# Kernel tuning notes

Hardware: AMD Instinct MI355X
Metric: run time of the kernel (lower is better)

The kernel has to match this reference:

```python
import jax, jax.numpy as jnp
import numpy as np

N = 100_000        # node_num
E_RAND = 1_600_000 # random edges; self-loops appended (PyG add_self_loops=True)
F_IN = 128         # n_xdims
HEADS = 8          # gat_nhead
F_HID = 8          # GATConv out_channels of layer 1
SLOPE = 0.2        # PyG GATConv default negative_slope


def _gat_layer(x, src, dst, W, a_src, a_dst, bias, heads, out_dim, n):
    # x: [N, Fin], W: [Fin, heads*out_dim], a_*: [heads, out_dim], bias: [heads*out_dim]
    h = (x @ W).reshape(n, heads, out_dim)                 # [N, H, D]
    s = jnp.sum(h * a_src, axis=-1)                        # [N, H] per-node src term
    d = jnp.sum(h * a_dst, axis=-1)                        # [N, H] per-node dst term
    e = jax.nn.leaky_relu(s[src] + d[dst], SLOPE)          # [E, H] edge logits
    # segment softmax over incoming edges of each destination node
    m = jax.ops.segment_max(e, dst, num_segments=n)        # [N, H]
    ex = jnp.exp(e - m[dst])                               # [E, H]
    denom = jax.ops.segment_sum(ex, dst, num_segments=n)   # [N, H]
    alpha = ex / denom[dst]                                # [E, H]
    msg = h[src] * alpha[:, :, None]                       # [E, H, D]
    out = jax.ops.segment_sum(msg, dst, num_segments=n)    # [N, H, D]
    return out.reshape(n, heads * out_dim) + bias          # concat=True


def setup_inputs() -> dict:
    key = jax.random.key(0)
    ks = jax.random.split(key, 10)
    x = jax.random.normal(ks[0], (N, F_IN), dtype=jnp.float32)
    ei = jax.random.randint(ks[1], (2, E_RAND), 0, N, dtype=jnp.int64)
    loops = jnp.broadcast_to(jnp.arange(N, dtype=jnp.int64), (2, N))
    edge_index = jnp.concatenate([ei, loops], axis=1)      # [2, E_RAND + N]
    g1 = 1.0 / np.sqrt(F_IN)
    g2 = 1.0 / np.sqrt(HEADS * F_HID)
    return {
        "x": x,
        "edge_index": edge_index,
        "W1": jax.random.normal(ks[2], (F_IN, HEADS * F_HID), dtype=jnp.float32) * g1,
        "a_src1": jax.random.normal(ks[3], (HEADS, F_HID), dtype=jnp.float32) * g2,
        "a_dst1": jax.random.normal(ks[4], (HEADS, F_HID), dtype=jnp.float32) * g2,
        "b1": jnp.zeros((HEADS * F_HID,), dtype=jnp.float32),
        "W2": jax.random.normal(ks[5], (HEADS * F_HID, F_IN), dtype=jnp.float32) * g2,
        "a_src2": jax.random.normal(ks[6], (1, F_IN), dtype=jnp.float32) * (1.0 / np.sqrt(F_IN)),
        "a_dst2": jax.random.normal(ks[7], (1, F_IN), dtype=jnp.float32) * (1.0 / np.sqrt(F_IN)),
        "b2": jnp.zeros((F_IN,), dtype=jnp.float32),
    }


def reference(x, edge_index, W1, a_src1, a_dst1, b1, W2, a_src2, a_dst2, b2):
    src, dst = edge_index[0], edge_index[1]
    h = _gat_layer(x, src, dst, W1, a_src1, a_dst1, b1, HEADS, F_HID, N)
    h = jax.nn.relu(h)
    out = _gat_layer(h, src, dst, W2, a_src2, a_dst2, b2, 1, F_IN, N)
    return out
```

## Files before the change

kernel.cpp:

```cpp
#include <hip/hip_runtime.h>
#include <math.h>


#define SORT_EPB 4096

static __device__ __forceinline__ float lrelu(float v) {
    return v > 0.f ? v : 0.2f * v;
}

__global__ __launch_bounds__(64) void k_w2a(const float* __restrict__ W2,
                                            const float* __restrict__ as2,
                                            const float* __restrict__ ad2,
                                            float* __restrict__ w2as,
                                            float* __restrict__ w2ad) {
    int k = threadIdx.x;
    const float* row = W2 + k * 128;
    float s = 0.f, d = 0.f;
    #pragma unroll 8
    for (int j = 0; j < 128; ++j) { s = fmaf(row[j], as2[j], s); d = fmaf(row[j], ad2[j], d); }
    w2as[k] = s; w2ad[k] = d;
}

__global__ __launch_bounds__(256) void k_scan_blocks(const int* __restrict__ deg,
                                                     int* __restrict__ offs,
                                                     int* __restrict__ bsum, int N) {
    __shared__ int ls[256];
    const int t = threadIdx.x;
    const int base = blockIdx.x * 1024 + t * 4;
    int v0 = (base + 0 < N) ? deg[base + 0] : 0;
    int v1 = (base + 1 < N) ? deg[base + 1] : 0;
    int v2 = (base + 2 < N) ? deg[base + 2] : 0;
    int v3 = (base + 3 < N) ? deg[base + 3] : 0;
    const int sum = v0 + v1 + v2 + v3;
    int val = sum;
    ls[t] = val;
    __syncthreads();
    for (int off = 1; off < 256; off <<= 1) {
        int x = (t >= off) ? ls[t - off] : 0;
        __syncthreads();
        val += x;
        ls[t] = val;
        __syncthreads();
    }
    int run = val - sum;
    if (base + 0 < N) offs[base + 0] = run;  run += v0;
    if (base + 1 < N) offs[base + 1] = run;  run += v1;
    if (base + 2 < N) offs[base + 2] = run;  run += v2;
    if (base + 3 < N) offs[base + 3] = run;
    if (t == 255) bsum[blockIdx.x] = val;
}

__global__ __launch_bounds__(256) void k_scan_tops(int* __restrict__ bsum, int B) {
    __shared__ int ls[256];
    const int t = threadIdx.x;
    int v = (t < B) ? bsum[t] : 0;
    int val = v;
    ls[t] = val;
    __syncthreads();
    for (int off = 1; off < 256; off <<= 1) {
        int x = (t >= off) ? ls[t - off] : 0;
        __syncthreads();
        val += x;
        ls[t] = val;
        __syncthreads();
    }
    if (t < B) bsum[t] = val - v;
}

__global__ __launch_bounds__(256) void k_scan_add(int* __restrict__ offs,
                                                  const int* __restrict__ bsum,
                                                  int N, int E) {
    int i = blockIdx.x * 256 + threadIdx.x;
    if (i < N) offs[i] = offs[i] + bsum[i >> 10];
    if (i == 0) offs[N] = E;
}

__global__ __launch_bounds__(256) void k_hist(const int* __restrict__ dst,
                                              int* __restrict__ counts,
                                              int E, int B, int NB2) {
    __shared__ int h[256];
    const int t = threadIdx.x;
    const int b = blockIdx.x;
    h[t] = 0;
    __syncthreads();
    const int base_i = b * SORT_EPB;
    #pragma unroll 4
    for (int k = 0; k < 16; ++k) {
        int i = base_i + k * 256 + t;
        if (i < E) atomicAdd(&h[dst[i] >> 9], 1);
    }
    __syncthreads();
    if (t < NB2) counts[t * B + b] = h[t];
}

__global__ __launch_bounds__(256) void k_bucket_scatter(const int* __restrict__ src,
                                                        const int* __restrict__ dst,
                                                        const int* __restrict__ base,
                                                        int* __restrict__ packed,
                                                        int E, int B, int NB2) {
    __shared__ int cur[256];
    const int t = threadIdx.x;
    const int b = blockIdx.x;
    if (t < NB2) cur[t] = base[t * B + b];
    __syncthreads();
    const int base_i = b * SORT_EPB;
    #pragma unroll 4
    for (int k = 0; k < 16; ++k) {
        int i = base_i + k * 256 + t;
        if (i < E) {
            int d = dst[i];
            int pos = atomicAdd(&cur[d >> 9], 1);
            packed[pos] = (src[i] << 9) | (d & 511);
        }
    }
}

__global__ __launch_bounds__(256) void k_bucket_sort(const int* __restrict__ packed,
                                                     const int* __restrict__ base,
                                                     int* __restrict__ srcs,
                                                     int* __restrict__ offs,
                                                     int E, int B, int N) {
    __shared__ int h[512], sc[512], cur[512], ls[256];
    const int t = threadIdx.x;
    const int j = blockIdx.x;
    const int bstart = base[j * B];
    const int bend   = base[(j + 1) * B];
    h[t] = 0; h[t + 256] = 0;
    __syncthreads();
    for (int i = bstart + t; i < bend; i += 256)
        atomicAdd(&h[packed[i] & 511], 1);
    __syncthreads();
    const int a0 = h[2 * t], a1 = h[2 * t + 1];
    int val = a0 + a1;
    ls[t] = val;
    __syncthreads();
    for (int off = 1; off < 256; off <<= 1) {
        int x = (t >= off) ? ls[t - off] : 0;
        __syncthreads();
        val += x;
        ls[t] = val;
        __syncthreads();
    }
    const int pre = val - (a0 + a1);
    sc[2 * t] = pre;         sc[2 * t + 1] = pre + a0;
    cur[2 * t] = pre;        cur[2 * t + 1] = pre + a0;
    __syncthreads();
    const int node0 = j * 512 + 2 * t;
    if (node0 < N)     offs[node0]     = bstart + sc[2 * t];
    if (node0 + 1 < N) offs[node0 + 1] = bstart + sc[2 * t + 1];
    if (j == 0 && t == 0) offs[N] = E;
    for (int i = bstart + t; i < bend; i += 256) {
        int p = packed[i];
        int pos = atomicAdd(&cur[p & 511], 1);
        srcs[bstart + pos] = p >> 9;
    }
}

__global__ __launch_bounds__(256) void k_gemm1(const float* __restrict__ x,
                                               const float* __restrict__ W,
                                               const float* __restrict__ a_s,
                                               const float* __restrict__ a_d,
                                               float* __restrict__ h,
                                               float* __restrict__ s1,
                                               float* __restrict__ d1, int N) {
    __shared__ float Ws[128 * 64];
    __shared__ float xs[64][68];
    const int t = threadIdx.x;
    for (int i = t; i < 128 * 64; i += 256) Ws[i] = W[i];
    const int row0 = blockIdx.x * 64;
    const int tc = (t & 15) * 4;
    const int tr = (t >> 4) * 4;
    float acc[4][4] = {};
    for (int kb = 0; kb < 128; kb += 64) {
        if (kb) __syncthreads();
        for (int i = t; i < 1024; i += 256) {
            int r = i >> 4, c = i & 15;
            float4 v = make_float4(0.f, 0.f, 0.f, 0.f);
            if (row0 + r < N)
                v = *(const float4*)(x + (size_t)(row0 + r) * 128 + kb + c * 4);
            *(float4*)&xs[r][c * 4] = v;
        }
        __syncthreads();
        #pragma unroll 4
        for (int k = 0; k < 64; k += 4) {
            const float4 xv0 = *(const float4*)&xs[tr + 0][k];
            const float4 xv1 = *(const float4*)&xs[tr + 1][k];
            const float4 xv2 = *(const float4*)&xs[tr + 2][k];
            const float4 xv3 = *(const float4*)&xs[tr + 3][k];
            #pragma unroll
            for (int kk = 0; kk < 4; ++kk) {
                const float4 w = *(const float4*)&Ws[(kb + k + kk) * 64 + tc];
                const float a0 = (&xv0.x)[kk], a1 = (&xv1.x)[kk];
                const float a2 = (&xv2.x)[kk], a3 = (&xv3.x)[kk];
                acc[0][0] = fmaf(a0, w.x, acc[0][0]); acc[0][1] = fmaf(a0, w.y, acc[0][1]);
                acc[0][2] = fmaf(a0, w.z, acc[0][2]); acc[0][3] = fmaf(a0, w.w, acc[0][3]);
                acc[1][0] = fmaf(a1, w.x, acc[1][0]); acc[1][1] = fmaf(a1, w.y, acc[1][1]);
                acc[1][2] = fmaf(a1, w.z, acc[1][2]); acc[1][3] = fmaf(a1, w.w, acc[1][3]);
                acc[2][0] = fmaf(a2, w.x, acc[2][0]); acc[2][1] = fmaf(a2, w.y, acc[2][1]);
                acc[2][2] = fmaf(a2, w.z, acc[2][2]); acc[2][3] = fmaf(a2, w.w, acc[2][3]);
                acc[3][0] = fmaf(a3, w.x, acc[3][0]); acc[3][1] = fmaf(a3, w.y, acc[3][1]);
                acc[3][2] = fmaf(a3, w.z, acc[3][2]); acc[3][3] = fmaf(a3, w.w, acc[3][3]);
            }
        }
    }
    #pragma unroll
    for (int i = 0; i < 4; ++i) {
        int r = row0 + tr + i;
        if (r < N)
            *(float4*)(h + (size_t)r * 64 + tc) =
                make_float4(acc[i][0], acc[i][1], acc[i][2], acc[i][3]);
    }
    const float as0 = a_s[tc + 0], as1v = a_s[tc + 1], as2v = a_s[tc + 2], as3 = a_s[tc + 3];
    const float ad0 = a_d[tc + 0], ad1v = a_d[tc + 1], ad2v = a_d[tc + 2], ad3 = a_d[tc + 3];
    #pragma unroll
    for (int i = 0; i < 4; ++i) {
        float ps = acc[i][0] * as0 + acc[i][1] * as1v + acc[i][2] * as2v + acc[i][3] * as3;
        float pd = acc[i][0] * ad0 + acc[i][1] * ad1v + acc[i][2] * ad2v + acc[i][3] * ad3;
        ps += __shfl_xor(ps, 1);
        pd += __shfl_xor(pd, 1);
        int r = row0 + tr + i;
        if ((t & 1) == 0 && r < N) {
            int hh = (t & 15) >> 1;
            s1[r * 8 + hh] = ps;
            d1[r * 8 + hh] = pd;
        }
    }
}

__global__ __launch_bounds__(256) void k_gemm_out(const float* __restrict__ u,
                                                  const float* __restrict__ W,
                                                  const float* __restrict__ bias,
                                                  float* __restrict__ out, int N) {
    __shared__ float Ws[64 * 128];
    __shared__ float xs[32][68];
    const int t = threadIdx.x;
    for (int i = t; i < 64 * 128; i += 256) Ws[i] = W[i];
    const int row0 = blockIdx.x * 32;
    for (int i = t; i < 512; i += 256) {
        int r = i >> 4, c = i & 15;
        float4 v = make_float4(0.f, 0.f, 0.f, 0.f);
        if (row0 + r < N)
            v = *(const float4*)(u + (size_t)(row0 + r) * 64 + c * 4);
        *(float4*)&xs[r][c * 4] = v;
    }
    __syncthreads();
    const int tc = (t & 31) * 4;
    const int tr = (t >> 5) * 4;
    float acc[4][4] = {};
    #pragma unroll 4
    for (int k = 0; k < 64; k += 4) {
        const float4 xv0 = *(const float4*)&xs[tr + 0][k];
        const float4 xv1 = *(const float4*)&xs[tr + 1][k];
        const float4 xv2 = *(const float4*)&xs[tr + 2][k];
        const float4 xv3 = *(const float4*)&xs[tr + 3][k];
        #pragma unroll
        for (int kk = 0; kk < 4; ++kk) {
            const float4 w = *(const float4*)&Ws[(k + kk) * 128 + tc];
            const float a0 = (&xv0.x)[kk], a1 = (&xv1.x)[kk];
            const float a2 = (&xv2.x)[kk], a3 = (&xv3.x)[kk];
            acc[0][0] = fmaf(a0, w.x, acc[0][0]); acc[0][1] = fmaf(a0, w.y, acc[0][1]);
            acc[0][2] = fmaf(a0, w.z, acc[0][2]); acc[0][3] = fmaf(a0, w.w, acc[0][3]);
            acc[1][0] = fmaf(a1, w.x, acc[1][0]); acc[1][1] = fmaf(a1, w.y, acc[1][1]);
            acc[1][2] = fmaf(a1, w.z, acc[1][2]); acc[1][3] = fmaf(a1, w.w, acc[1][3]);
            acc[2][0] = fmaf(a2, w.x, acc[2][0]); acc[2][1] = fmaf(a2, w.y, acc[2][1]);
            acc[2][2] = fmaf(a2, w.z, acc[2][2]); acc[2][3] = fmaf(a2, w.w, acc[2][3]);
            acc[3][0] = fmaf(a3, w.x, acc[3][0]); acc[3][1] = fmaf(a3, w.y, acc[3][1]);
            acc[3][2] = fmaf(a3, w.z, acc[3][2]); acc[3][3] = fmaf(a3, w.w, acc[3][3]);
        }
    }
    const float4 bv = *(const float4*)(bias + tc);
    #pragma unroll
    for (int i = 0; i < 4; ++i) {
        int r = row0 + tr + i;
        if (r < N)
            *(float4*)(out + (size_t)r * 128 + tc) =
                make_float4(acc[i][0] + bv.x, acc[i][1] + bv.y,
                            acc[i][2] + bv.z, acc[i][3] + bv.w);
    }
}

__global__ __launch_bounds__(256) void k_agg1(const float* __restrict__ h1,
                                              const float* __restrict__ s1,
                                              const float* __restrict__ d1,
                                              const int* __restrict__ offs,
                                              const int* __restrict__ srcs,
                                              const float* __restrict__ bias,
                                              const float* __restrict__ w2as,
                                              const float* __restrict__ w2ad,
                                              float* __restrict__ out,
                                              float* __restrict__ s2,
                                              float* __restrict__ d2, int N) {
    int wid = (blockIdx.x * 256 + threadIdx.x) >> 6;
    int lane = threadIdx.x & 63;
    if (wid >= N) return;
    const int beg = offs[wid], end = offs[wid + 1];
    const int slot = lane >> 3;
    const int hl = lane & 7;
    const int c = lane & 31;
    const int half = lane >> 5;
    const int hc = c >> 2;
    const float dt = d1[wid * 8 + hl];
    float accx = 0.f, accy = 0.f, dsum = 0.f;
    int sa = 0, sb = 0; float exa = 0.f, exb = 0.f;
    if (beg + slot < end)     { sa = srcs[beg + slot];     exa = __expf(lrelu(s1[sa * 8 + hl] + dt)); }
    if (beg + 8 + slot < end) { sb = srcs[beg + 8 + slot]; exb = __expf(lrelu(s1[sb * 8 + hl] + dt)); }
    for (int cb = beg; cb < end; cb += 16) {
        int sna = 0, snb = 0; float exna = 0.f, exnb = 0.f;
        if (cb + 16 + slot < end) { sna = srcs[cb + 16 + slot]; exna = __expf(lrelu(s1[sna * 8 + hl] + dt)); }
        if (cb + 24 + slot < end) { snb = srcs[cb + 24 + slot]; exnb = __expf(lrelu(s1[snb * 8 + hl] + dt)); }
        dsum += exa + exb;
        #pragma unroll
        for (int p = 0; p < 4; ++p) {
            const int sl = (2 * p + half) * 8;
            const float e0 = __shfl(exa, sl + hc);
            const int  ss0 = __shfl(sa, sl);
            const float e1 = __shfl(exb, sl + hc);
            const int  ss1 = __shfl(sb, sl);
            const float2 hv0 = *(const float2*)(h1 + (size_t)ss0 * 64 + 2 * c);
            const float2 hv1 = *(const float2*)(h1 + (size_t)ss1 * 64 + 2 * c);
            accx = fmaf(hv0.x, e0, accx); accy = fmaf(hv0.y, e0, accy);
            accx = fmaf(hv1.x, e1, accx); accy = fmaf(hv1.y, e1, accy);
        }
        sa = sna; exa = exna; sb = snb; exb = exnb;
    }
    accx += __shfl_xor(accx, 32);
    accy += __shfl_xor(accy, 32);
    dsum += __shfl_xor(dsum, 8);
    dsum += __shfl_xor(dsum, 16);
    dsum += __shfl_xor(dsum, 32);
    const float denom = __shfl(dsum, hc);
    float ox = 0.f, oy = 0.f;
    if (half == 0) {
        const float2 bv = *(const float2*)(bias + 2 * c);
        ox = fmaxf(accx / denom + bv.x, 0.f);
        oy = fmaxf(accy / denom + bv.y, 0.f);
        *(float2*)(out + (size_t)wid * 64 + 2 * c) = make_float2(ox, oy);
    }
    float ps = 0.f, pd = 0.f;
    if (half == 0) {
        const float2 was = *(const float2*)(w2as + 2 * c);
        const float2 wad = *(const float2*)(w2ad + 2 * c);
        ps = ox * was.x + oy * was.y;
        pd = ox * wad.x + oy * wad.y;
    }
    #pragma unroll
    for (int mask = 1; mask < 32; mask <<= 1) {
        ps += __shfl_xor(ps, mask);
        pd += __shfl_xor(pd, mask);
    }
    if (lane == 0) { s2[wid] = ps; d2[wid] = pd; }
}

__global__ __launch_bounds__(256) void k_agg2(const float* __restrict__ hrelu,
                                              const float* __restrict__ s2,
                                              const float* __restrict__ d2,
                                              const int* __restrict__ offs,
                                              const int* __restrict__ srcs,
                                              float* __restrict__ u, int N) {
    int wid = (blockIdx.x * 256 + threadIdx.x) >> 6;
    int lane = threadIdx.x & 63;
    if (wid >= N) return;
    const int beg = offs[wid], end = offs[wid + 1];
    const int c = lane & 31;
    const int half = lane >> 5;
    const float dn = d2[wid];
    float accx = 0.f, accy = 0.f, dsum = 0.f;
    int s_cur = 0; float ex_cur = 0.f;
    if (beg + lane < end) {
        s_cur = srcs[beg + lane];
        ex_cur = __expf(lrelu(s2[s_cur] + dn));
    }
    for (int cb = beg; cb < end; cb += 64) {
        int sn = 0; float exn = 0.f;
        if (cb + 64 + lane < end) { sn = srcs[cb + 64 + lane]; exn = __expf(lrelu(s2[sn] + dn)); }
        dsum += ex_cur;
        const int npairs = (min(64, end - cb) + 1) >> 1;
        for (int p0 = 0; p0 < npairs; p0 += 8) {
            #pragma unroll
            for (int q = 0; q < 8; ++q) {
                const int sl = min(2 * (p0 + q) + half, 63);
                const float e = __shfl(ex_cur, sl);
                const int ss = __shfl(s_cur, sl);
                const float2 hv = *(const float2*)(hrelu + (size_t)ss * 64 + 2 * c);
                accx = fmaf(hv.x, e, accx);
                accy = fmaf(hv.y, e, accy);
            }
        }
        s_cur = sn; ex_cur = exn;
    }
    accx += __shfl_xor(accx, 32);
    accy += __shfl_xor(accy, 32);
    #pragma unroll
    for (int mask = 1; mask < 64; mask <<= 1) dsum += __shfl_xor(dsum, mask);
    if (half == 0) {
        const float inv = 1.f / dsum;
        *(float2*)(u + (size_t)wid * 64 + 2 * c) = make_float2(accx * inv, accy * inv);
    }
}


extern "C" void kernel_launch(void* const* d_in, const int* in_sizes, int n_in,
                              void* d_out, int out_size, void* d_ws, size_t ws_size,
                              hipStream_t stream) {
    const float* x   = (const float*)d_in[0];
    const int*   ei  = (const int*)d_in[1];
    const float* W1  = (const float*)d_in[2];
    const float* as1 = (const float*)d_in[3];
    const float* ad1 = (const float*)d_in[4];
    const float* b1  = (const float*)d_in[5];
    const float* W2  = (const float*)d_in[6];
    const float* as2 = (const float*)d_in[7];
    const float* ad2 = (const float*)d_in[8];
    const float* b2  = (const float*)d_in[9];
    float* out = (float*)d_out;

    const int N = in_sizes[0] / 128;
    const int E = in_sizes[1] / 2;
    const int* srcp = ei;
    const int* dstp = ei + E;

    const int SB  = (E + SORT_EPB - 1) / SORT_EPB;
    const int NB2 = (N + 511) >> 9;
    const int L   = NB2 * SB;

    char* w = (char*)d_ws;
    auto carve = [&](size_t bytes) -> char* {
        char* p = w;
        w += (bytes + 255) & ~(size_t)255;
        return p;
    };
    float* h1    = (float*)carve((size_t)N * 64 * 4);
    float* hrelu = (float*)carve((size_t)N * 64 * 4);
    float* u     = (float*)carve((size_t)N * 64 * 4);
    float* s1    = (float*)carve((size_t)N * 8 * 4);
    float* d1    = (float*)carve((size_t)N * 8 * 4);
    float* s2    = (float*)carve((size_t)N * 4);
    float* d2    = (float*)carve((size_t)N * 4);
    float* w2as  = (float*)carve(64 * 4);
    float* w2ad  = (float*)carve(64 * 4);
    int*   offs  = (int*)carve((size_t)(N + 1) * 4);
    int*   counts= (int*)carve((size_t)(L + 1) * 4);
    const int BS = (L + 1023) / 1024;
    int*   bsum  = (int*)carve((size_t)BS * 4);
    int*   packed= (int*)carve((size_t)E * 4);
    int*   srcs  = (int*)carve((size_t)E * 4);
    (void)ws_size; (void)n_in; (void)out_size;

    const int TB = 256;
    hipLaunchKernelGGL(k_w2a, dim3(1), dim3(64), 0, stream, W2, as2, ad2, w2as, w2ad);
    hipLaunchKernelGGL(k_hist,           dim3(SB), dim3(TB), 0, stream, dstp, counts, E, SB, NB2);
    hipLaunchKernelGGL(k_scan_blocks,    dim3(BS), dim3(TB), 0, stream, counts, counts, bsum, L);
    hipLaunchKernelGGL(k_scan_tops,      dim3(1),  dim3(TB), 0, stream, bsum, BS);
    hipLaunchKernelGGL(k_scan_add,       dim3((L + TB - 1) / TB), dim3(TB), 0, stream, counts, bsum, L, E);
    hipLaunchKernelGGL(k_bucket_scatter, dim3(SB), dim3(TB), 0, stream, srcp, dstp, counts, packed, E, SB, NB2);
    hipLaunchKernelGGL(k_bucket_sort,    dim3(NB2), dim3(TB), 0, stream, packed, counts, srcs, offs, E, SB, N);
    hipLaunchKernelGGL(k_gemm1, dim3((N + 63) / 64), dim3(TB), 0, stream, x, W1, as1, ad1, h1, s1, d1, N);
    hipLaunchKernelGGL(k_agg1,  dim3((N + 3) / 4),   dim3(TB), 0, stream,
                       h1, s1, d1, offs, srcs, b1, w2as, w2ad, hrelu, s2, d2, N);
    hipLaunchKernelGGL(k_agg2,     dim3((N + 3) / 4),   dim3(TB), 0, stream, hrelu, s2, d2, offs, srcs, u, N);
    hipLaunchKernelGGL(k_gemm_out, dim3((N + 31) / 32), dim3(TB), 0, stream, u, W2, b2, out, N);
}
```

Measured before the change: 395.0 us.

## Fuse output GEMM into agg2, fold w2a into hist, batch gather loads

Removes the separate output GEMM kernel: each wavefront in agg2 now multiplies its normalized 64-wide aggregate by W2 via shuffles and writes the 128-wide output row directly, dropping the u intermediate buffer. The tiny W2·a projection kernel becomes an extra block of the histogram kernel, saving a launch. The gather loops in agg1 and agg2 are restructured to issue all shuffles, then all loads, then all FMAs, so more memory requests are in flight at once. The cost is that W2 is read from global/L2 per wavefront instead of from shared memory.

Result: slower. 438.3 us (+11.0%).

```diff
diff --git a/kernel.cpp b/kernel.cpp
--- a/kernel.cpp
+++ b/kernel.cpp
@@ -6,19 +6,6 @@
 
 static __device__ __forceinline__ float lrelu(float v) {
     return v > 0.f ? v : 0.2f * v;
-}
-
-__global__ __launch_bounds__(64) void k_w2a(const float* __restrict__ W2,
-                                            const float* __restrict__ as2,
-                                            const float* __restrict__ ad2,
-                                            float* __restrict__ w2as,
-                                            float* __restrict__ w2ad) {
-    int k = threadIdx.x;
-    const float* row = W2 + k * 128;
-    float s = 0.f, d = 0.f;
-    #pragma unroll 8
-    for (int j = 0; j < 128; ++j) { s = fmaf(row[j], as2[j], s); d = fmaf(row[j], ad2[j], d); }
-    w2as[k] = s; w2ad[k] = d;
 }
 
 __global__ __launch_bounds__(256) void k_scan_blocks(const int* __restrict__ deg,
@@ -77,10 +64,25 @@
 
 __global__ __launch_bounds__(256) void k_hist(const int* __restrict__ dst,
                                               int* __restrict__ counts,
-                                              int E, int B, int NB2) {
+                                              int E, int B, int NB2,
+                                              const float* __restrict__ W2,
+                                              const float* __restrict__ as2,
+                                              const float* __restrict__ ad2,
+                                              float* __restrict__ w2as,
+                                              float* __restrict__ w2ad) {
+    const int t = threadIdx.x;
+    const int b = blockIdx.x;
+    if (b == B) {
+        if (t < 64) {
+            const float* row = W2 + t * 128;
+            float s = 0.f, d = 0.f;
+            #pragma unroll 8
+            for (int j = 0; j < 128; ++j) { s = fmaf(row[j], as2[j], s); d = fmaf(row[j], ad2[j], d); }
+            w2as[t] = s; w2ad[t] = d;
+        }
+        return;
+    }
     __shared__ int h[256];
-    const int t = threadIdx.x;
-    const int b = blockIdx.x;
     h[t] = 0;
     __syncthreads();
     const int base_i = b * SORT_EPB;
@@ -224,58 +226,6 @@
             s1[r * 8 + hh] = ps;
             d1[r * 8 + hh] = pd;
         }
-    }
-}
-
-__global__ __launch_bounds__(256) void k_gemm_out(const float* __restrict__ u,
-                                                  const float* __restrict__ W,
-                                                  const float* __restrict__ bias,
-                                                  float* __restrict__ out, int N) {
-    __shared__ float Ws[64 * 128];
-    __shared__ float xs[32][68];
-    const int t = threadIdx.x;
-    for (int i = t; i < 64 * 128; i += 256) Ws[i] = W[i];
-    const int row0 = blockIdx.x * 32;
-    for (int i = t; i < 512; i += 256) {
-        int r = i >> 4, c = i & 15;
-        float4 v = make_float4(0.f, 0.f, 0.f, 0.f);
-        if (row0 + r < N)
-            v = *(const float4*)(u + (size_t)(row0 + r) * 64 + c * 4);
-        *(float4*)&xs[r][c * 4] = v;
-    }
-    __syncthreads();
-    const int tc = (t & 31) * 4;
-    const int tr = (t >> 5) * 4;
-    float acc[4][4] = {};
-    #pragma unroll 4
-    for (int k = 0; k < 64; k += 4) {
-        const float4 xv0 = *(const float4*)&xs[tr + 0][k];
-        const float4 xv1 = *(const float4*)&xs[tr + 1][k];
-        const float4 xv2 = *(const float4*)&xs[tr + 2][k];
-        const float4 xv3 = *(const float4*)&xs[tr + 3][k];
-        #pragma unroll
-        for (int kk = 0; kk < 4; ++kk) {
-            const float4 w = *(const float4*)&Ws[(k + kk) * 128 + tc];
-            const float a0 = (&xv0.x)[kk], a1 = (&xv1.x)[kk];
-            const float a2 = (&xv2.x)[kk], a3 = (&xv3.x)[kk];
-            acc[0][0] = fmaf(a0, w.x, acc[0][0]); acc[0][1] = fmaf(a0, w.y, acc[0][1]);
-            acc[0][2] = fmaf(a0, w.z, acc[0][2]); acc[0][3] = fmaf(a0, w.w, acc[0][3]);
-            acc[1][0] = fmaf(a1, w.x, acc[1][0]); acc[1][1] = fmaf(a1, w.y, acc[1][1]);
-            acc[1][2] = fmaf(a1, w.z, acc[1][2]); acc[1][3] = fmaf(a1, w.w, acc[1][3]);
-            acc[2][0] = fmaf(a2, w.x, acc[2][0]); acc[2][1] = fmaf(a2, w.y, acc[2][1]);
-            acc[2][2] = fmaf(a2, w.z, acc[2][2]); acc[2][3] = fmaf(a2, w.w, acc[2][3]);
-            acc[3][0] = fmaf(a3, w.x, acc[3][0]); acc[3][1] = fmaf(a3, w.y, acc[3][1]);
-            acc[3][2] = fmaf(a3, w.z, acc[3][2]); acc[3][3] = fmaf(a3, w.w, acc[3][3]);
-        }
-    }
-    const float4 bv = *(const float4*)(bias + tc);
-    #pragma unroll
-    for (int i = 0; i < 4; ++i) {
-        int r = row0 + tr + i;
-        if (r < N)
-            *(float4*)(out + (size_t)r * 128 + tc) =
-                make_float4(acc[i][0] + bv.x, acc[i][1] + bv.y,
-                            acc[i][2] + bv.z, acc[i][3] + bv.w);
     }
 }
 
@@ -309,17 +259,23 @@
         if (cb + 16 + slot < end) { sna = srcs[cb + 16 + slot]; exna = __expf(lrelu(s1[sna * 8 + hl] + dt)); }
         if (cb + 24 + slot < end) { snb = srcs[cb + 24 + slot]; exnb = __expf(lrelu(s1[snb * 8 + hl] + dt)); }
         dsum += exa + exb;
+        int ssA[4], ssB[4]; float eA[4], eB[4];
         #pragma unroll
         for (int p = 0; p < 4; ++p) {
             const int sl = (2 * p + half) * 8;
-            const float e0 = __shfl(exa, sl + hc);
-            const int  ss0 = __shfl(sa, sl);
-            const float e1 = __shfl(exb, sl + hc);
-            const int  ss1 = __shfl(sb, sl);
-            const float2 hv0 = *(const float2*)(h1 + (size_t)ss0 * 64 + 2 * c);
-            const float2 hv1 = *(const float2*)(h1 + (size_t)ss1 * 64 + 2 * c);
-            accx = fmaf(hv0.x, e0, accx); accy = fmaf(hv0.y, e0, accy);
-            accx = fmaf(hv1.x, e1, accx); accy = fmaf(hv1.y, e1, accy);
+            eA[p] = __shfl(exa, sl + hc);  ssA[p] = __shfl(sa, sl);
+            eB[p] = __shfl(exb, sl + hc);  ssB[p] = __shfl(sb, sl);
+        }
+        float2 hA[4], hB[4];
+        #pragma unroll
+        for (int p = 0; p < 4; ++p) {
+            hA[p] = *(const float2*)(h1 + (size_t)ssA[p] * 64 + 2 * c);
+            hB[p] = *(const float2*)(h1 + (size_t)ssB[p] * 64 + 2 * c);
+        }
+        #pragma unroll
+        for (int p = 0; p < 4; ++p) {
+            accx = fmaf(hA[p].x, eA[p], accx); accy = fmaf(hA[p].y, eA[p], accy);
+            accx = fmaf(hB[p].x, eB[p], accx); accy = fmaf(hB[p].y, eB[p], accy);
         }
         sa = sna; exa = exna; sb = snb; exb = exnb;
     }
@@ -356,7 +312,9 @@
                                               const float* __restrict__ d2,
                                               const int* __restrict__ offs,
                                               const int* __restrict__ srcs,
-                                              float* __restrict__ u, int N) {
+                                              const float* __restrict__ W2,
+                                              const float* __restrict__ b2,
+                                              float* __restrict__ out, int N) {
     int wid = (blockIdx.x * 256 + threadIdx.x) >> 6;
     int lane = threadIdx.x & 63;
     if (wid >= N) return;
@@ -376,14 +334,21 @@
         dsum += ex_cur;
         const int npairs = (min(64, end - cb) + 1) >> 1;
         for (int p0 = 0; p0 < npairs; p0 += 8) {
+            int ss[8]; float e[8];
             #pragma unroll
             for (int q = 0; q < 8; ++q) {
                 const int sl = min(2 * (p0 + q) + half, 63);
-                const float e = __shfl(ex_cur, sl);
-                const int ss = __shfl(s_cur, sl);
-                const float2 hv = *(const float2*)(hrelu + (size_t)ss * 64 + 2 * c);
-                accx = fmaf(hv.x, e, accx);
-                accy = fmaf(hv.y, e, accy);
+                e[q] = __shfl(ex_cur, sl);
+                ss[q] = __shfl(s_cur, sl);
+            }
+            float2 hv[8];
+            #pragma unroll
+            for (int q = 0; q < 8; ++q)
+                hv[q] = *(const float2*)(hrelu + (size_t)ss[q] * 64 + 2 * c);
+            #pragma unroll
+            for (int q = 0; q < 8; ++q) {
+                accx = fmaf(hv[q].x, e[q], accx);
+                accy = fmaf(hv[q].y, e[q], accy);
             }
         }
         s_cur = sn; ex_cur = exn;
@@ -392,10 +357,22 @@
     accy += __shfl_xor(accy, 32);
     #pragma unroll
     for (int mask = 1; mask < 64; mask <<= 1) dsum += __shfl_xor(dsum, mask);
-    if (half == 0) {
-        const float inv = 1.f / dsum;
-        *(float2*)(u + (size_t)wid * 64 + 2 * c) = make_float2(accx * inv, accy * inv);
-    }
+    const float inv = 1.f / dsum;
+    const float ux = accx * inv;
+    const float uy = accy * inv;
+    float o0 = 0.f, o1 = 0.f;
+    #pragma unroll 8
+    for (int k2 = 0; k2 < 32; ++k2) {
+        const float vx = __shfl(ux, k2);
+        const float vy = __shfl(uy, k2);
+        const float* w0 = W2 + (2 * k2) * 128;
+        o0 = fmaf(vx, w0[lane], o0);
+        o1 = fmaf(vx, w0[lane + 64], o1);
+        o0 = fmaf(vy, w0[128 + lane], o0);
+        o1 = fmaf(vy, w0[128 + lane + 64], o1);
+    }
+    out[(size_t)wid * 128 + lane]      = o0 + b2[lane];
+    out[(size_t)wid * 128 + 64 + lane] = o1 + b2[lane + 64];
 }
 
 
@@ -431,7 +408,6 @@
     };
     float* h1    = (float*)carve((size_t)N * 64 * 4);
     float* hrelu = (float*)carve((size_t)N * 64 * 4);
-    float* u     = (float*)carve((size_t)N * 64 * 4);
     float* s1    = (float*)carve((size_t)N * 8 * 4);
     float* d1    = (float*)carve((size_t)N * 8 * 4);
     float* s2    = (float*)carve((size_t)N * 4);
@@ -447,8 +423,8 @@
     (void)ws_size; (void)n_in; (void)out_size;
 
     const int TB = 256;
-    hipLaunchKernelGGL(k_w2a, dim3(1), dim3(64), 0, stream, W2, as2, ad2, w2as, w2ad);
-    hipLaunchKernelGGL(k_hist,           dim3(SB), dim3(TB), 0, stream, dstp, counts, E, SB, NB2);
+    hipLaunchKernelGGL(k_hist,           dim3(SB + 1), dim3(TB), 0, stream,
+                       dstp, counts, E, SB, NB2, W2, as2, ad2, w2as, w2ad);
     hipLaunchKernelGGL(k_scan_blocks,    dim3(BS), dim3(TB), 0, stream, counts, counts, bsum, L);
     hipLaunchKernelGGL(k_scan_tops,      dim3(1),  dim3(TB), 0, stream, bsum, BS);
     hipLaunchKernelGGL(k_scan_add,       dim3((L + TB - 1) / TB), dim3(TB), 0, stream, counts, bsum, L, E);
@@ -457,6 +433,6 @@
     hipLaunchKernelGGL(k_gemm1, dim3((N + 63) / 64), dim3(TB), 0, stream, x, W1, as1, ad1, h1, s1, d1, N);
     hipLaunchKernelGGL(k_agg1,  dim3((N + 3) / 4),   dim3(TB), 0, stream,
                        h1, s1, d1, offs, srcs, b1, w2as, w2ad, hrelu, s2, d2, N);
-    hipLaunchKernelGGL(k_agg2,     dim3((N + 3) / 4),   dim3(TB), 0, stream, hrelu, s2, d2, offs, srcs, u, N);
-    hipLaunchKernelGGL(k_gemm_out, dim3((N + 31) / 32), dim3(TB), 0, stream, u, W2, b2, out, N);
-}
+    hipLaunchKernelGGL(k_agg2, dim3((N + 3) / 4), dim3(TB), 0, stream,
+                       hrelu, s2, d2, offs, srcs, W2, b2, out, N);
+}
```
